# Kernel tuning notes

Hardware: AMD Instinct MI355X
Metric: run time of the kernel (lower is better)

Reference implementation:

```python
import jax, jax.numpy as jnp
import numpy as np
import math

B, T, D, H = 2, 2048, 2048, 16
HD = D // H  # head_dim = 128


def setup_inputs() -> dict:
    key = jax.random.key(0)
    ks = jax.random.split(key, 9)
    s = 1.0 / math.sqrt(D)
    return {
        "x": jax.random.normal(ks[0], (B, T, D), dtype=jnp.float32),
        "Wq": jax.random.normal(ks[1], (D, D), dtype=jnp.float32) * s,
        "bq": jax.random.normal(ks[2], (D,), dtype=jnp.float32) * 0.01,
        "Wk": jax.random.normal(ks[3], (D, D), dtype=jnp.float32) * s,
        "bk": jax.random.normal(ks[4], (D,), dtype=jnp.float32) * 0.01,
        "Wv": jax.random.normal(ks[5], (D, D), dtype=jnp.float32) * s,
        "bv": jax.random.normal(ks[6], (D,), dtype=jnp.float32) * 0.01,
        "Wo": jax.random.normal(ks[7], (D, D), dtype=jnp.float32) * s,
        "bo": jax.random.normal(ks[8], (D,), dtype=jnp.float32) * 0.01,
    }


def reference(x, Wq, bq, Wk, bk, Wv, bv, Wo, bo):
    b, t, c = x.shape
    # projections; split heads: (B,T,D) -> (B,H,T,HD)
    def split_heads(y):
        return y.reshape(b, t, H, HD).transpose(0, 2, 1, 3)

    q = split_heads(x @ Wq + bq)
    k = split_heads(x @ Wk + bk)
    v = split_heads(x @ Wv + bv)

    scale = 1.0 / math.sqrt(HD)
    attn = jnp.einsum('bhqd,bhkd->bhqk', q, k) * scale  # (B,H,T,T)
    # causal mask (prefill path: past_k is None)
    causal = jnp.tril(jnp.ones((t, t), dtype=bool))
    attn = jnp.where(causal, attn, -jnp.inf)
    attn = jax.nn.softmax(attn, axis=-1)
    out = jnp.einsum('bhqk,bhkd->bhqd', attn, v)  # (B,H,T,HD)
    out = out.transpose(0, 2, 1, 3).reshape(b, t, c)
    out = out @ Wo + bo
    return (out, k, v)
```

## Files before the change

kernel.cpp:

```cpp
#include <hip/hip_runtime.h>
#include <hip/hip_bf16.h>

#define B_ 2
#define T_ 2048
#define D_ 2048
#define H_ 16
#define HD_ 128
#define M_ 4096

typedef __attribute__((ext_vector_type(8))) short short8;
typedef __attribute__((ext_vector_type(8))) __bf16 bf16x8;
typedef __attribute__((ext_vector_type(4))) float f32x4;
typedef __attribute__((ext_vector_type(4))) unsigned uint32x4;

__device__ __forceinline__ short f2bf(float f) {
  unsigned u = __builtin_bit_cast(unsigned, f);
  u += 0x7fffu + ((u >> 16) & 1u);
  return (short)(u >> 16);
}

__device__ __forceinline__ unsigned pk2(float lo, float hi) {
  return ((unsigned)(unsigned short)f2bf(hi) << 16) |
         (unsigned)(unsigned short)f2bf(lo);
}

__device__ __forceinline__ void gl_lds16(const void* g, void* l) {
  __builtin_amdgcn_global_load_lds(
      (const __attribute__((address_space(1))) unsigned int*)g,
      (__attribute__((address_space(3))) unsigned int*)l, 16, 0, 0);
}

__device__ __forceinline__ f32x4 mfma_bf16(short8 a, short8 b, f32x4 c) {
  return __builtin_amdgcn_mfma_f32_16x16x32_bf16(
      __builtin_bit_cast(bf16x8, a), __builtin_bit_cast(bf16x8, b), c, 0, 0, 0);
}

__device__ __forceinline__ float2 sw16f(float x) {
  float a = x, bv;
  asm("v_mov_b32 %0, %1" : "=v"(bv) : "v"(x));
  asm("v_permlane16_swap_b32 %0, %1" : "+v"(a), "+v"(bv));
  return make_float2(a, bv);
}
__device__ __forceinline__ float2 sw32f(float x) {
  float a = x, bv;
  asm("v_mov_b32 %0, %1" : "=v"(bv) : "v"(x));
  asm("v_permlane32_swap_b32 %0, %1" : "+v"(a), "+v"(bv));
  return make_float2(a, bv);
}
__device__ __forceinline__ void sw16u(unsigned x, unsigned& e, unsigned& o) {
  unsigned a = x, bv;
  asm("v_mov_b32 %0, %1" : "=v"(bv) : "v"(x));
  asm("v_permlane16_swap_b32 %0, %1" : "+v"(a), "+v"(bv));
  e = a; o = bv;
}
__device__ __forceinline__ void pl32u(unsigned& a, unsigned& b) {
  asm("v_permlane32_swap_b32 %0, %1" : "+v"(a), "+v"(b));
}

__global__ void cast_f32_bf16(const float* __restrict__ in, short* __restrict__ out, int n4) {
  int i = blockIdx.x * blockDim.x + threadIdx.x;
  int stride = gridDim.x * blockDim.x;
  for (; i < n4; i += stride) {
    float4 v = ((const float4*)in)[i];
    short4 s;
    s.x = f2bf(v.x); s.y = f2bf(v.y); s.z = f2bf(v.z); s.w = f2bf(v.w);
    ((short4*)out)[i] = s;
  }
}

__global__ void transpose_cast_w4(const float* __restrict__ Wq, const float* __restrict__ Wk,
                                  const float* __restrict__ Wv, const float* __restrict__ Wo,
                                  short* __restrict__ wqkv, short* __restrict__ wo) {
  __shared__ float t[32][33];
  int z = blockIdx.z;
  const float* W = z == 0 ? Wq : z == 1 ? Wk : z == 2 ? Wv : Wo;
  short* dst = z < 3 ? wqkv + (size_t)z * D_ * D_ : wo;
  int n0 = blockIdx.x * 32, k0 = blockIdx.y * 32;
  int tx = threadIdx.x, ty = threadIdx.y;
#pragma unroll
  for (int j = 0; j < 4; ++j)
    t[ty + j * 8][tx] = W[(size_t)(k0 + ty + j * 8) * D_ + n0 + tx];
  __syncthreads();
#pragma unroll
  for (int j = 0; j < 4; ++j)
    dst[(size_t)(n0 + ty + j * 8) * D_ + k0 + tx] = f2bf(t[tx][ty + j * 8]);
}

__global__ __launch_bounds__(512, 2) void gemm_qkv(
    const short* __restrict__ A, const short* __restrict__ Bt,
    const float* __restrict__ b0, const float* __restrict__ b1,
    const float* __restrict__ b2,
    short* __restrict__ q_o, short* __restrict__ k_o,
    float* __restrict__ kf_o, float* __restrict__ vf_o,
    short* __restrict__ vt_o) {
  __shared__ __attribute__((aligned(16))) char lds[2][57344];
  const int K = D_, NT = K / 64;

  int d = blockIdx.x;
  int lg = (d & 7) * 64 + (d >> 3);
  int m0 = (lg & 15) * 256, n0 = (lg >> 4) * 192;

  int tid = threadIdx.x, lane = tid & 63, wid = tid >> 6;
  int wm = wid >> 2, wn = wid & 3;
  int lr = lane & 15, g = lane >> 4;

  int rowA = tid >> 2;
  int cA = ((((tid & 3) << 4) ^ (((rowA >> 1) & 3) << 4)) >> 1);
  const short* aS = A + (size_t)(m0 + rowA) * K + cA;
  int rowB = tid >> 3;
  int cB = ((((tid & 7) << 4) ^ ((rowB & 7) << 4)) >> 1);
  const short* bS = Bt + (size_t)(n0 + rowB) * K + cB;
  char* ldsb = (char*)lds;

  auto stageA = [&](int ts, int kh) {
    char* dst = ldsb + (ts & 1) * 57344 + kh * 16384 + tid * 16;
    const short* s = aS + ts * 64 + kh * 32;
    gl_lds16(s, dst);
    gl_lds16(s + (size_t)128 * K, dst + 8192);
  };
  auto stageB = [&](int ts) {
    char* dst = ldsb + (ts & 1) * 57344 + 32768 + tid * 16;
    const short* s = bS + ts * 64;
    gl_lds16(s, dst);
    gl_lds16(s + (size_t)64 * K, dst + 8192);
    gl_lds16(s + (size_t)128 * K, dst + 16384);
  };

  int swzA = (g * 16) ^ (((lr >> 1) & 3) << 4);
  int aoff = (wm * 128 + lr) * 64 + swzA;
  int boff0 = (wn * 48 + lr) * 128 + ((g * 16) ^ ((lr & 7) << 4));
  int boff1 = (wn * 48 + lr) * 128 + (((64 + g * 16)) ^ ((lr & 7) << 4));

  f32x4 acc[8][3] = {};

  stageA(0, 0); stageB(0); stageA(0, 1); stageA(1, 0);
  asm volatile("s_waitcnt vmcnt(4)" ::: "memory");
  __builtin_amdgcn_s_barrier();
  __builtin_amdgcn_sched_barrier(0);

#pragma unroll 1
  for (int t = 0; t < NT; ++t) {
    const char* base = ldsb + (t & 1) * 57344;
    int t1 = (t + 1 < NT) ? t + 1 : NT - 1;
    int t2 = (t + 2 < NT) ? t + 2 : NT - 1;
    short8 afr[8], bfr[3];

#pragma unroll
    for (int mi = 0; mi < 8; ++mi) afr[mi] = *(const short8*)(base + aoff + mi * 1024);
#pragma unroll
    for (int ni = 0; ni < 3; ++ni) bfr[ni] = *(const short8*)(base + 32768 + boff0 + ni * 2048);
    stageA(t1, 1); stageB(t1);
    __builtin_amdgcn_s_setprio(1);
#pragma unroll
    for (int mi = 0; mi < 8; ++mi)
#pragma unroll
      for (int ni = 0; ni < 3; ++ni)
        acc[mi][ni] = mfma_bf16(afr[mi], bfr[ni], acc[mi][ni]);
    __builtin_amdgcn_s_setprio(0);
    asm volatile("s_waitcnt vmcnt(7)" ::: "memory");
    __builtin_amdgcn_s_barrier();
    __builtin_amdgcn_sched_barrier(0);

#pragma unroll
    for (int mi = 0; mi < 8; ++mi) afr[mi] = *(const short8*)(base + 16384 + aoff + mi * 1024);
#pragma unroll
    for (int ni = 0; ni < 3; ++ni) bfr[ni] = *(const short8*)(base + 32768 + boff1 + ni * 2048);
    stageA(t2, 0);
    __builtin_amdgcn_s_setprio(1);
#pragma unroll
    for (int mi = 0; mi < 8; ++mi)
#pragma unroll
      for (int ni = 0; ni < 3; ++ni)
        acc[mi][ni] = mfma_bf16(afr[mi], bfr[ni], acc[mi][ni]);
    __builtin_amdgcn_s_setprio(0);
    asm volatile("s_waitcnt vmcnt(2)" ::: "memory");
    __builtin_amdgcn_s_barrier();
    __builtin_amdgcn_sched_barrier(0);
  }

#pragma unroll
  for (int ni = 0; ni < 3; ++ni) {
    int gcb = n0 + wn * 48 + ni * 16;
    int region = gcb >> 11;
    int nc = (gcb & 2047) + lr;
    int hh = nc >> 7, hd = nc & 127;
    const float* bias = region == 0 ? b0 : region == 1 ? b1 : b2;
    float bv = bias[nc];
#pragma unroll
    for (int mi = 0; mi < 8; ++mi) {
      int gr0 = m0 + wm * 128 + mi * 16 + (g << 2);
      int bb = gr0 >> 11, tt0 = gr0 & 2047;
      size_t hbase = (size_t)(bb * H_ + hh);
      float v0 = acc[mi][ni][0] + bv;
      float v1 = acc[mi][ni][1] + bv;
      float v2 = acc[mi][ni][2] + bv;
      float v3 = acc[mi][ni][3] + bv;
      size_t ib = (hbase * T_ + tt0) * HD_ + hd;
      if (region == 0) {
        q_o[ib] = f2bf(v0); q_o[ib + HD_] = f2bf(v1);
        q_o[ib + 2 * HD_] = f2bf(v2); q_o[ib + 3 * HD_] = f2bf(v3);
      } else if (region == 1) {
        k_o[ib] = f2bf(v0); k_o[ib + HD_] = f2bf(v1);
        k_o[ib + 2 * HD_] = f2bf(v2); k_o[ib + 3 * HD_] = f2bf(v3);
        kf_o[ib] = v0; kf_o[ib + HD_] = v1;
        kf_o[ib + 2 * HD_] = v2; kf_o[ib + 3 * HD_] = v3;
      } else {
        vf_o[ib] = v0; vf_o[ib + HD_] = v1;
        vf_o[ib + 2 * HD_] = v2; vf_o[ib + 3 * HD_] = v3;
        short4 s4;
        s4.x = f2bf(v0); s4.y = f2bf(v1); s4.z = f2bf(v2); s4.w = f2bf(v3);
        *(short4*)&vt_o[(hbase * HD_ + hd) * T_ + tt0] = s4;
      }
    }
  }
}

__global__ __launch_bounds__(256, 2) void gemm_rb(
    const short* __restrict__ A, const short* __restrict__ Bt,
    const float* __restrict__ b0, float* __restrict__ f_o) {
  __shared__ __attribute__((aligned(16))) short lds[4][2][4096];
  const int K = D_, NT = K / 32;

  int nx = gridDim.x, nwg = nx * gridDim.y;
  int d = blockIdx.y * nx + blockIdx.x;
  int cpx = nwg >> 3;
  int lg = (d & 7) * cpx + (d >> 3);
  int m0 = (lg / nx) * 128, n0 = (lg % nx) * 128;

  int tid = threadIdx.x, lane = tid & 63, w = tid >> 6;
  int wm = w >> 1, wn = w & 1;
  int lr = lane & 15, g = lane >> 4;

  int o1 = tid * 16, o2 = 4096 + tid * 16;
  int row1 = tid >> 2, row2 = 64 + row1;
  int cb = (tid & 3) << 4;
  int c1 = (cb ^ (((row1 >> 1) & 3) << 4)) >> 1;
  int c2 = (cb ^ (((row2 >> 1) & 3) << 4)) >> 1;
  const short* aS1 = A + (size_t)(m0 + row1) * K + c1;
  const short* aS2 = A + (size_t)(m0 + row2) * K + c2;
  const short* bS1 = Bt + (size_t)(n0 + row1) * K + c1;
  const short* bS2 = Bt + (size_t)(n0 + row2) * K + c2;

  int aoff[4], boff[4];
#pragma unroll
  for (int i = 0; i < 4; ++i) {
    int ra = wm * 64 + i * 16 + lr;
    aoff[i] = ra * 64 + ((g * 16) ^ (((ra >> 1) & 3) << 4));
    int rb = wn * 64 + i * 16 + lr;
    boff[i] = rb * 64 + ((g * 16) ^ (((rb >> 1) & 3) << 4));
  }

  f32x4 acc[4][4] = {};

#pragma unroll
  for (int s = 0; s < 3; ++s) {
    char* la = (char*)&lds[s][0][0];
    char* lb = (char*)&lds[s][1][0];
    gl_lds16(aS1 + s * 32, la + o1);
    gl_lds16(aS2 + s * 32, la + o2);
    gl_lds16(bS1 + s * 32, lb + o1);
    gl_lds16(bS2 + s * 32, lb + o2);
  }
  asm volatile("s_waitcnt vmcnt(8)" ::: "memory");
  __builtin_amdgcn_s_barrier();
  __builtin_amdgcn_sched_barrier(0);

#pragma unroll 1
  for (int t4 = 0; t4 < NT; t4 += 4) {
#pragma unroll
    for (int p = 0; p < 4; ++p) {
      int t = t4 + p;
      {
        int ts = (t + 3 < NT) ? t + 3 : NT - 1;
        char* la = (char*)&lds[(p + 3) & 3][0][0];
        char* lb = (char*)&lds[(p + 3) & 3][1][0];
        gl_lds16(aS1 + ts * 32, la + o1);
        gl_lds16(aS2 + ts * 32, la + o2);
        gl_lds16(bS1 + ts * 32, lb + o1);
        gl_lds16(bS2 + ts * 32, lb + o2);
      }
      const char* la = (const char*)&lds[p][0][0];
      const char* lb = (const char*)&lds[p][1][0];
      short8 af[4], bfv[4];
#pragma unroll
      for (int i = 0; i < 4; ++i) {
        af[i] = *(const short8*)(la + aoff[i]);
        bfv[i] = *(const short8*)(lb + boff[i]);
      }
      __builtin_amdgcn_s_setprio(1);
#pragma unroll
      for (int mi = 0; mi < 4; ++mi)
#pragma unroll
        for (int ni = 0; ni < 4; ++ni)
          acc[mi][ni] = mfma_bf16(af[mi], bfv[ni], acc[mi][ni]);
      __builtin_amdgcn_s_setprio(0);
      asm volatile("s_waitcnt vmcnt(8)" ::: "memory");
      __builtin_amdgcn_s_barrier();
      __builtin_amdgcn_sched_barrier(0);
    }
  }

#pragma unroll
  for (int mi = 0; mi < 4; ++mi) {
#pragma unroll
    for (int ni = 0; ni < 4; ++ni) {
      int gr0 = m0 + wm * 64 + mi * 16 + (g << 2);
      int gc = n0 + wn * 64 + ni * 16 + lr;
      float bv = b0[gc];
#pragma unroll
      for (int r = 0; r < 4; ++r)
        f_o[(size_t)(gr0 + r) * D_ + gc] = acc[mi][ni][r] + bv;
    }
  }
}

__global__ __launch_bounds__(256, 2) void attn_fwd(
    const short* __restrict__ qb, const short* __restrict__ kb,
    const short* __restrict__ vtb, short* __restrict__ aob) {
  __shared__ __attribute__((aligned(16))) char kvlds[2][16384];

  int d = blockIdx.y * gridDim.x + blockIdx.x;
  int lg = (d & 7) * 64 + (d >> 3);
  int bh = lg >> 4, jx = lg & 15;

  int tid = threadIdx.x, w = tid >> 6, lane = tid & 63;
  int lr = lane & 15, g = lane >> 4;
  const short* Q  = qb  + (size_t)bh * T_ * HD_;
  const short* Kp = kb  + (size_t)bh * T_ * HD_;
  const short* Vt = vtb + (size_t)bh * HD_ * T_;
  const float scale = 0.08838834764831845f;
  int b = bh >> 4, h = bh & 15;
  bool hi16 = (lane & 16) != 0;

  int oA = ((2 * w + 0) * 64 + lane) * 16;
  int oB = ((2 * w + 1) * 64 + lane) * 16;
  int rKA = oA >> 8, rKB = oB >> 8;
  size_t skA = (size_t)rKA * HD_ + (((oA & 255) ^ ((rKA & 7) << 4)) >> 1);
  size_t skB = (size_t)rKB * HD_ + (((oB & 255) ^ ((rKB & 7) << 4)) >> 1);
  int rVA = oA >> 6, rVB = oB >> 6;
  size_t svA = (size_t)rVA * T_ + (((oA & 63) ^ (((rVA >> 1) & 3) << 4)) >> 1);
  size_t svB = (size_t)rVB * T_ + (((oB & 63) ^ (((rVB >> 1) & 3) << 4)) >> 1);

#pragma unroll 1
  for (int pass = 0; pass < 2; ++pass) {
    int qt = pass ? (31 - jx) : jx;
    int q0 = qt * 64 + w * 16;
    int ntiles = 2 * qt + 2;

    {
      char* kd = &kvlds[0][0];
      char* vd = &kvlds[0][8192];
      gl_lds16(Kp + skA, kd + oA);
      gl_lds16(Kp + skB, kd + oB);
      gl_lds16(Vt + svA, vd + oA);
      gl_lds16(Vt + svB, vd + oB);
    }

    short8 qf[4];
#pragma unroll
    for (int kk = 0; kk < 4; ++kk)
      qf[kk] = *(const short8*)&Q[(size_t)(q0 + lr) * HD_ + kk * 32 + g * 8];

    f32x4 o[8] = {};
    float mrow = -1e30f, lrow = 0.f;
    __syncthreads();

#pragma unroll 1
    for (int t = 0; t < ntiles; ++t) {
      int kv0 = t * 32, buf = t & 1;
      if (t + 1 < ntiles) {
        char* kd = &kvlds[buf ^ 1][0];
        char* vd = &kvlds[buf ^ 1][8192];
        const short* Kn = Kp + (size_t)(kv0 + 32) * HD_;
        const short* Vn = Vt + (kv0 + 32);
        gl_lds16(Kn + skA, kd + oA);
        gl_lds16(Kn + skB, kd + oB);
        gl_lds16(Vn + svA, vd + oA);
        gl_lds16(Vn + svB, vd + oB);
      }
      if (kv0 < q0 + 16) {
        const char* kb_ = &kvlds[buf][0];
        const char* vb_ = &kvlds[buf][8192];
        short8 kf0[4], kf1[4], vf[8];
#pragma unroll
        for (int kk = 0; kk < 4; ++kk) {
          int cs = (kk * 64 + g * 16) ^ ((lr & 7) << 4);
          kf0[kk] = *(const short8*)(kb_ + (lr * 256 + cs));
          kf1[kk] = *(const short8*)(kb_ + ((16 + lr) * 256 + cs));
        }
#pragma unroll
        for (int f = 0; f < 8; ++f)
          vf[f] = *(const short8*)(vb_ + ((f * 16 + lr) * 64 +
                   ((g * 16) ^ (((lr >> 1) & 3) << 4))));

        f32x4 s0 = {}, s1 = {};
        __builtin_amdgcn_s_setprio(1);
#pragma unroll
        for (int kk = 0; kk < 4; ++kk) {
          s0 = mfma_bf16(kf0[kk], qf[kk], s0);
          s1 = mfma_bf16(kf1[kk], qf[kk], s1);
        }
        __builtin_amdgcn_s_setprio(0);

        float vv[8];
#pragma unroll
        for (int r = 0; r < 4; ++r) {
          vv[r] = s0[r] * scale;
          vv[4 + r] = s1[r] * scale;
        }
        if (kv0 + 31 > q0) {
          int qrow = q0 + lr;
#pragma unroll
          for (int r = 0; r < 4; ++r) {
            if (kv0 + 4 * g + r > qrow) vv[r] = -1e30f;
            if (kv0 + 16 + 4 * g + r > qrow) vv[4 + r] = -1e30f;
          }
        }

        float pm = vv[0];
#pragma unroll
        for (int i = 1; i < 8; ++i) pm = fmaxf(pm, vv[i]);
        { float2 tpm = sw32f(pm); pm = fmaxf(tpm.x, tpm.y); }
        { float2 tpm = sw16f(pm); pm = fmaxf(tpm.x, tpm.y); }

        bool rescale = !__all(pm - mrow <= 8.0f);
        float alpha = 1.0f;
        if (rescale) {
          float mnew = fmaxf(mrow, pm);
          alpha = __expf(mrow - mnew);
          mrow = mnew;
        }

        float p[8];
        float rs = 0.f;
#pragma unroll
        for (int i = 0; i < 8; ++i) { p[i] = __expf(vv[i] - mrow); rs += p[i]; }
        { float2 trs = sw32f(rs); rs = trs.x + trs.y; }
        { float2 trs = sw16f(rs); rs = trs.x + trs.y; }
        lrow = (rescale ? lrow * alpha : lrow) + rs;

        if (rescale) {
          float alr[4];
#pragma unroll
          for (int r = 0; r < 4; ++r) alr[r] = __shfl(alpha, 4 * g + r);
#pragma unroll
          for (int f = 0; f < 8; ++f)
#pragma unroll
            for (int r = 0; r < 4; ++r) o[f][r] *= alr[r];
        }

        unsigned w0 = pk2(p[0], p[1]), w1 = pk2(p[2], p[3]);
        unsigned w2 = pk2(p[4], p[5]), w3 = pk2(p[6], p[7]);
        unsigned e0, od0, e1, od1, e2, od2, e3, od3;
        sw16u(w0, e0, od0); sw16u(w1, e1, od1);
        sw16u(w2, e2, od2); sw16u(w3, e3, od3);
        unsigned F0 = e0,  S0 = e2;  pl32u(F0, S0);
        unsigned F1 = e1,  S1 = e3;  pl32u(F1, S1);
        unsigned F2 = od0, S2 = od2; pl32u(F2, S2);
        unsigned F3 = od1, S3 = od3; pl32u(F3, S3);
        uint32x4 paw = { hi16 ? S0 : F0, hi16 ? S1 : F1,
                         hi16 ? S2 : F2, hi16 ? S3 : F3 };
        short8 pa = __builtin_bit_cast(short8, paw);

        __builtin_amdgcn_s_setprio(1);
#pragma unroll
        for (int f = 0; f < 8; ++f) o[f] = mfma_bf16(pa, vf[f], o[f]);
        __builtin_amdgcn_s_setprio(0);
      }
      __syncthreads();
    }

    float inv = 1.0f / lrow;
    float invr[4];
#pragma unroll
    for (int r = 0; r < 4; ++r) invr[r] = __shfl(inv, 4 * g + r);
#pragma unroll
    for (int r = 0; r < 4; ++r) {
      int q = q0 + 4 * g + r;
      size_t rowoff = ((size_t)(b * T_ + q)) * D_ + h * HD_;
#pragma unroll
      for (int f = 0; f < 8; ++f)
        aob[rowoff + f * 16 + lr] = f2bf(o[f][r] * invr[r]);
    }
  }
}

extern "C" void kernel_launch(void* const* d_in, const int* in_sizes, int n_in,
                              void* d_out, int out_size, void* d_ws, size_t ws_size,
                              hipStream_t stream) {
  const float* x  = (const float*)d_in[0];
  const float* Wq = (const float*)d_in[1];
  const float* bq = (const float*)d_in[2];
  const float* Wk = (const float*)d_in[3];
  const float* bk = (const float*)d_in[4];
  const float* Wv = (const float*)d_in[5];
  const float* bv = (const float*)d_in[6];
  const float* Wo = (const float*)d_in[7];
  const float* bo = (const float*)d_in[8];
  float* out  = (float*)d_out;
  float* kout = out + (size_t)M_ * D_;
  float* vout = kout + (size_t)M_ * D_;

  char* ws = (char*)d_ws;
  auto alloc = [&](size_t bytes) {
    char* p = ws;
    ws += (bytes + 255) & ~(size_t)255;
    return p;
  };
  short* xb    = (short*)alloc((size_t)M_ * D_ * 2);
  short* wqkvT = (short*)alloc((size_t)3 * D_ * D_ * 2);
  short* woT   = (short*)alloc((size_t)D_ * D_ * 2);
  short* qb    = (short*)alloc((size_t)M_ * D_ * 2);
  short* kb    = (short*)alloc((size_t)M_ * D_ * 2);
  short* vtb   = (short*)alloc((size_t)M_ * D_ * 2);
  short* aob = xb;

  cast_f32_bf16<<<2048, 256, 0, stream>>>(x, xb, M_ * D_ / 4);
  dim3 tb(32, 8);
  transpose_cast_w4<<<dim3(64, 64, 4), tb, 0, stream>>>(Wq, Wk, Wv, Wo, wqkvT, woT);

  gemm_qkv<<<512, 512, 0, stream>>>(xb, wqkvT, bq, bk, bv, qb, kb, kout, vout, vtb);
  attn_fwd<<<dim3(16, 32), 256, 0, stream>>>(qb, kb, vtb, aob);
  gemm_rb<<<dim3(16, 32), 256, 0, stream>>>(aob, woT, bo, out);
}
```

Before: 256.4 us.

## Split GEMM k-step into four interleaved phases and use hardware bf16 pack

Restructures the projection GEMM main loop so each half-k step is split into two sub-phases of 4 M-fragments. LDS fragment loads and global-to-LDS staging are interleaved with barriers, and the vmcnt waits are retuned to match the new issue order. The aim is to cut register pressure from holding 8 A fragments and to overlap MFMA with staging at finer grain, at the cost of more barriers per iteration. Separately, the attention P-to-bf16 packing swaps the software round-to-nearest for the v_cvt_pk_bf16_f32 instruction.

```diff
diff --git a/kernel.cpp b/kernel.cpp
--- a/kernel.cpp
+++ b/kernel.cpp
@@ -19,9 +19,10 @@
   return (short)(u >> 16);
 }
 
-__device__ __forceinline__ unsigned pk2(float lo, float hi) {
-  return ((unsigned)(unsigned short)f2bf(hi) << 16) |
-         (unsigned)(unsigned short)f2bf(lo);
+__device__ __forceinline__ unsigned cvtpk(float lo, float hi) {
+  unsigned r;
+  asm("v_cvt_pk_bf16_f32 %0, %1, %2" : "=v"(r) : "v"(lo), "v"(hi));
+  return r;
 }
 
 __device__ __forceinline__ void gl_lds16(const void* g, void* l) {
@@ -129,12 +130,12 @@
   int swzA = (g * 16) ^ (((lr >> 1) & 3) << 4);
   int aoff = (wm * 128 + lr) * 64 + swzA;
   int boff0 = (wn * 48 + lr) * 128 + ((g * 16) ^ ((lr & 7) << 4));
-  int boff1 = (wn * 48 + lr) * 128 + (((64 + g * 16)) ^ ((lr & 7) << 4));
+  int boff1 = (wn * 48 + lr) * 128 + ((64 + g * 16) ^ ((lr & 7) << 4));
 
   f32x4 acc[8][3] = {};
 
-  stageA(0, 0); stageB(0); stageA(0, 1); stageA(1, 0);
-  asm volatile("s_waitcnt vmcnt(4)" ::: "memory");
+  stageA(0, 0); stageA(0, 1); stageB(0); stageA(1, 0);
+  asm volatile("s_waitcnt vmcnt(2)" ::: "memory");
   __builtin_amdgcn_s_barrier();
   __builtin_amdgcn_sched_barrier(0);
 
@@ -143,35 +144,71 @@
     const char* base = ldsb + (t & 1) * 57344;
     int t1 = (t + 1 < NT) ? t + 1 : NT - 1;
     int t2 = (t + 2 < NT) ? t + 2 : NT - 1;
-    short8 afr[8], bfr[3];
-
-#pragma unroll
-    for (int mi = 0; mi < 8; ++mi) afr[mi] = *(const short8*)(base + aoff + mi * 1024);
+    short8 afr[4], bfr[3];
+
+#pragma unroll
+    for (int mi = 0; mi < 4; ++mi) afr[mi] = *(const short8*)(base + aoff + mi * 1024);
 #pragma unroll
     for (int ni = 0; ni < 3; ++ni) bfr[ni] = *(const short8*)(base + 32768 + boff0 + ni * 2048);
-    stageA(t1, 1); stageB(t1);
+    stageA(t1, 1);
+    __builtin_amdgcn_s_barrier();
+    asm volatile("s_waitcnt lgkmcnt(0)" ::: "memory");
+    __builtin_amdgcn_sched_barrier(0);
     __builtin_amdgcn_s_setprio(1);
 #pragma unroll
-    for (int mi = 0; mi < 8; ++mi)
+    for (int mi = 0; mi < 4; ++mi)
 #pragma unroll
       for (int ni = 0; ni < 3; ++ni)
         acc[mi][ni] = mfma_bf16(afr[mi], bfr[ni], acc[mi][ni]);
     __builtin_amdgcn_s_setprio(0);
-    asm volatile("s_waitcnt vmcnt(7)" ::: "memory");
-    __builtin_amdgcn_s_barrier();
-    __builtin_amdgcn_sched_barrier(0);
-
-#pragma unroll
-    for (int mi = 0; mi < 8; ++mi) afr[mi] = *(const short8*)(base + 16384 + aoff + mi * 1024);
+    __builtin_amdgcn_s_barrier();
+    __builtin_amdgcn_sched_barrier(0);
+
+#pragma unroll
+    for (int mi = 0; mi < 4; ++mi) afr[mi] = *(const short8*)(base + aoff + (4 + mi) * 1024);
+    stageB(t1);
+    __builtin_amdgcn_s_barrier();
+    asm volatile("s_waitcnt lgkmcnt(0)" ::: "memory");
+    __builtin_amdgcn_sched_barrier(0);
+    __builtin_amdgcn_s_setprio(1);
+#pragma unroll
+    for (int mi = 0; mi < 4; ++mi)
+#pragma unroll
+      for (int ni = 0; ni < 3; ++ni)
+        acc[4 + mi][ni] = mfma_bf16(afr[mi], bfr[ni], acc[4 + mi][ni]);
+    __builtin_amdgcn_s_setprio(0);
+    __builtin_amdgcn_s_barrier();
+    __builtin_amdgcn_sched_barrier(0);
+
+#pragma unroll
+    for (int mi = 0; mi < 4; ++mi) afr[mi] = *(const short8*)(base + 16384 + aoff + mi * 1024);
 #pragma unroll
     for (int ni = 0; ni < 3; ++ni) bfr[ni] = *(const short8*)(base + 32768 + boff1 + ni * 2048);
     stageA(t2, 0);
+    __builtin_amdgcn_s_barrier();
+    asm volatile("s_waitcnt lgkmcnt(0)" ::: "memory");
+    __builtin_amdgcn_sched_barrier(0);
     __builtin_amdgcn_s_setprio(1);
 #pragma unroll
-    for (int mi = 0; mi < 8; ++mi)
+    for (int mi = 0; mi < 4; ++mi)
 #pragma unroll
       for (int ni = 0; ni < 3; ++ni)
         acc[mi][ni] = mfma_bf16(afr[mi], bfr[ni], acc[mi][ni]);
+    __builtin_amdgcn_s_setprio(0);
+    __builtin_amdgcn_s_barrier();
+    __builtin_amdgcn_sched_barrier(0);
+
+#pragma unroll
+    for (int mi = 0; mi < 4; ++mi) afr[mi] = *(const short8*)(base + 16384 + aoff + (4 + mi) * 1024);
+    __builtin_amdgcn_s_barrier();
+    asm volatile("s_waitcnt lgkmcnt(0)" ::: "memory");
+    __builtin_amdgcn_sched_barrier(0);
+    __builtin_amdgcn_s_setprio(1);
+#pragma unroll
+    for (int mi = 0; mi < 4; ++mi)
+#pragma unroll
+      for (int ni = 0; ni < 3; ++ni)
+        acc[4 + mi][ni] = mfma_bf16(afr[mi], bfr[ni], acc[4 + mi][ni]);
     __builtin_amdgcn_s_setprio(0);
     asm volatile("s_waitcnt vmcnt(2)" ::: "memory");
     __builtin_amdgcn_s_barrier();
@@ -449,8 +486,8 @@
             for (int r = 0; r < 4; ++r) o[f][r] *= alr[r];
         }
 
-        unsigned w0 = pk2(p[0], p[1]), w1 = pk2(p[2], p[3]);
-        unsigned w2 = pk2(p[4], p[5]), w3 = pk2(p[6], p[7]);
+        unsigned w0 = cvtpk(p[0], p[1]), w1 = cvtpk(p[2], p[3]);
+        unsigned w2 = cvtpk(p[4], p[5]), w3 = cvtpk(p[6], p[7]);
         unsigned e0, od0, e1, od1, e2, od2, e3, od3;
         sw16u(w0, e0, od0); sw16u(w1, e1, od1);
         sw16u(w2, e2, od2); sw16u(w3, e3, od3);
```

After: 255.1 us. About the same (-0.5%).

## Enlarge QKV GEMM tile to 512x192 with triple-buffered K=32 stages

Applied to the files above, without the earlier changes.

The QKV projection GEMM now uses 512x192 block tiles on 256 blocks, with 4x2 waves each computing 128x96. It streams K in 32-wide steps through a three-slot LDS ring instead of a double-buffered 64-wide one. The aim is more reuse per loaded tile and deeper prefetch, paid for with more accumulator registers and fewer blocks, which lowers occupancy and CU coverage. Separately, the bf16 packing in attention switches from software rounding to the hardware v_cvt_pk_bf16_f32 instruction, and idle waves issue dummy loads so the vmcnt counts stay uniform.

```diff
diff --git a/kernel.cpp b/kernel.cpp
--- a/kernel.cpp
+++ b/kernel.cpp
@@ -19,9 +19,10 @@
   return (short)(u >> 16);
 }
 
-__device__ __forceinline__ unsigned pk2(float lo, float hi) {
-  return ((unsigned)(unsigned short)f2bf(hi) << 16) |
-         (unsigned)(unsigned short)f2bf(lo);
+__device__ __forceinline__ unsigned cvtpk(float lo, float hi) {
+  unsigned r;
+  asm("v_cvt_pk_bf16_f32 %0, %1, %2" : "=v"(r) : "v"(lo), "v"(hi));
+  return r;
 }
 
 __device__ __forceinline__ void gl_lds16(const void* g, void* l) {
@@ -93,94 +94,88 @@
     short* __restrict__ q_o, short* __restrict__ k_o,
     float* __restrict__ kf_o, float* __restrict__ vf_o,
     short* __restrict__ vt_o) {
-  __shared__ __attribute__((aligned(16))) char lds[2][57344];
-  const int K = D_, NT = K / 64;
+  __shared__ __attribute__((aligned(16))) char lds[3 * 45056 + 2048];
+  const int K = D_, NT = K / 32;
 
   int d = blockIdx.x;
-  int lg = (d & 7) * 64 + (d >> 3);
-  int m0 = (lg & 15) * 256, n0 = (lg >> 4) * 192;
+  int lg = (d & 7) * 32 + (d >> 3);
+  int m0 = (lg & 7) * 512, n0 = (lg >> 3) * 192;
 
   int tid = threadIdx.x, lane = tid & 63, wid = tid >> 6;
-  int wm = wid >> 2, wn = wid & 3;
+  int wm = wid >> 1, wn = wid & 1;
   int lr = lane & 15, g = lane >> 4;
 
-  int rowA = tid >> 2;
-  int cA = ((((tid & 3) << 4) ^ (((rowA >> 1) & 3) << 4)) >> 1);
-  const short* aS = A + (size_t)(m0 + rowA) * K + cA;
-  int rowB = tid >> 3;
-  int cB = ((((tid & 7) << 4) ^ ((rowB & 7) << 4)) >> 1);
-  const short* bS = Bt + (size_t)(n0 + rowB) * K + cB;
+  int scol = ((((tid & 3) << 4) ^ (((tid >> 3) & 3) << 4)) >> 1);
+  const short* aS = A + (size_t)(m0 + (tid >> 2)) * K + scol;
+  const short* bS = Bt + (size_t)(n0 + (tid >> 2)) * K + scol;
   char* ldsb = (char*)lds;
-
-  auto stageA = [&](int ts, int kh) {
-    char* dst = ldsb + (ts & 1) * 57344 + kh * 16384 + tid * 16;
-    const short* s = aS + ts * 64 + kh * 32;
-    gl_lds16(s, dst);
-    gl_lds16(s + (size_t)128 * K, dst + 8192);
+  char* scratch = ldsb + 3 * 45056;
+
+  auto stage = [&](int ts, int slot) {
+    char* sl = ldsb + slot * 45056;
+    const short* sa = aS + ts * 32;
+#pragma unroll
+    for (int j = 0; j < 4; ++j)
+      gl_lds16(sa + (size_t)j * 128 * K, sl + j * 8192 + wid * 1024);
+    if (wid < 6) {
+      const short* sb = bS + ts * 32;
+      gl_lds16(sb, sl + 32768 + wid * 1024);
+      gl_lds16(sb + (size_t)96 * K, sl + 32768 + 6144 + wid * 1024);
+    } else {
+      gl_lds16(A + lane * 8, scratch + (wid - 6) * 1024);
+      gl_lds16(A + lane * 8, scratch + (wid - 6) * 1024);
+    }
   };
-  auto stageB = [&](int ts) {
-    char* dst = ldsb + (ts & 1) * 57344 + 32768 + tid * 16;
-    const short* s = bS + ts * 64;
-    gl_lds16(s, dst);
-    gl_lds16(s + (size_t)64 * K, dst + 8192);
-    gl_lds16(s + (size_t)128 * K, dst + 16384);
-  };
-
-  int swzA = (g * 16) ^ (((lr >> 1) & 3) << 4);
-  int aoff = (wm * 128 + lr) * 64 + swzA;
-  int boff0 = (wn * 48 + lr) * 128 + ((g * 16) ^ ((lr & 7) << 4));
-  int boff1 = (wn * 48 + lr) * 128 + (((64 + g * 16)) ^ ((lr & 7) << 4));
-
-  f32x4 acc[8][3] = {};
-
-  stageA(0, 0); stageB(0); stageA(0, 1); stageA(1, 0);
-  asm volatile("s_waitcnt vmcnt(4)" ::: "memory");
+
+  int fsw = (g * 16) ^ (((lr >> 1) & 3) << 4);
+  int aoff = (wm * 128 + lr) * 64 + fsw;
+  int boff = 32768 + (wn * 96 + lr) * 64 + fsw;
+
+  f32x4 acc[8][6] = {};
+
+  stage(0, 0);
+  stage(1, 1);
+  asm volatile("s_waitcnt vmcnt(6)" ::: "memory");
   __builtin_amdgcn_s_barrier();
   __builtin_amdgcn_sched_barrier(0);
 
+  int sR = 0, sW = 2;
 #pragma unroll 1
   for (int t = 0; t < NT; ++t) {
-    const char* base = ldsb + (t & 1) * 57344;
-    int t1 = (t + 1 < NT) ? t + 1 : NT - 1;
-    int t2 = (t + 2 < NT) ? t + 2 : NT - 1;
-    short8 afr[8], bfr[3];
-
-#pragma unroll
-    for (int mi = 0; mi < 8; ++mi) afr[mi] = *(const short8*)(base + aoff + mi * 1024);
-#pragma unroll
-    for (int ni = 0; ni < 3; ++ni) bfr[ni] = *(const short8*)(base + 32768 + boff0 + ni * 2048);
-    stageA(t1, 1); stageB(t1);
+    const char* sl = ldsb + sR * 45056;
+    short8 bfr[6], afr[4];
+#pragma unroll
+    for (int ni = 0; ni < 6; ++ni) bfr[ni] = *(const short8*)(sl + boff + ni * 1024);
+#pragma unroll
+    for (int mi = 0; mi < 4; ++mi) afr[mi] = *(const short8*)(sl + aoff + mi * 1024);
+    int ts = (t + 2 < NT) ? t + 2 : NT - 1;
+    stage(ts, sW);
     __builtin_amdgcn_s_setprio(1);
 #pragma unroll
-    for (int mi = 0; mi < 8; ++mi)
-#pragma unroll
-      for (int ni = 0; ni < 3; ++ni)
+    for (int mi = 0; mi < 4; ++mi)
+#pragma unroll
+      for (int ni = 0; ni < 6; ++ni)
         acc[mi][ni] = mfma_bf16(afr[mi], bfr[ni], acc[mi][ni]);
     __builtin_amdgcn_s_setprio(0);
-    asm volatile("s_waitcnt vmcnt(7)" ::: "memory");
+#pragma unroll
+    for (int mi = 0; mi < 4; ++mi) afr[mi] = *(const short8*)(sl + aoff + (4 + mi) * 1024);
+    __builtin_amdgcn_s_setprio(1);
+#pragma unroll
+    for (int mi = 0; mi < 4; ++mi)
+#pragma unroll
+      for (int ni = 0; ni < 6; ++ni)
+        acc[4 + mi][ni] = mfma_bf16(afr[mi], bfr[ni], acc[4 + mi][ni]);
+    __builtin_amdgcn_s_setprio(0);
+    asm volatile("s_waitcnt vmcnt(6)" ::: "memory");
     __builtin_amdgcn_s_barrier();
     __builtin_amdgcn_sched_barrier(0);
-
-#pragma unroll
-    for (int mi = 0; mi < 8; ++mi) afr[mi] = *(const short8*)(base + 16384 + aoff + mi * 1024);
-#pragma unroll
-    for (int ni = 0; ni < 3; ++ni) bfr[ni] = *(const short8*)(base + 32768 + boff1 + ni * 2048);
-    stageA(t2, 0);
-    __builtin_amdgcn_s_setprio(1);
-#pragma unroll
-    for (int mi = 0; mi < 8; ++mi)
-#pragma unroll
-      for (int ni = 0; ni < 3; ++ni)
-        acc[mi][ni] = mfma_bf16(afr[mi], bfr[ni], acc[mi][ni]);
-    __builtin_amdgcn_s_setprio(0);
-    asm volatile("s_waitcnt vmcnt(2)" ::: "memory");
-    __builtin_amdgcn_s_barrier();
-    __builtin_amdgcn_sched_barrier(0);
-  }
-
-#pragma unroll
-  for (int ni = 0; ni < 3; ++ni) {
-    int gcb = n0 + wn * 48 + ni * 16;
+    sR = (sR == 2) ? 0 : sR + 1;
+    sW = (sW == 2) ? 0 : sW + 1;
+  }
+
+#pragma unroll
+  for (int ni = 0; ni < 6; ++ni) {
+    int gcb = n0 + wn * 96 + ni * 16;
     int region = gcb >> 11;
     int nc = (gcb & 2047) + lr;
     int hh = nc >> 7, hd = nc & 127;
@@ -449,8 +444,8 @@
             for (int r = 0; r < 4; ++r) o[f][r] *= alr[r];
         }
 
-        unsigned w0 = pk2(p[0], p[1]), w1 = pk2(p[2], p[3]);
-        unsigned w2 = pk2(p[4], p[5]), w3 = pk2(p[6], p[7]);
+        unsigned w0 = cvtpk(p[0], p[1]), w1 = cvtpk(p[2], p[3]);
+        unsigned w2 = cvtpk(p[4], p[5]), w3 = cvtpk(p[6], p[7]);
         unsigned e0, od0, e1, od1, e2, od2, e3, od3;
         sw16u(w0, e0, od0); sw16u(w1, e1, od1);
         sw16u(w2, e2, od2); sw16u(w3, e3, od3);
@@ -519,7 +514,7 @@
   dim3 tb(32, 8);
   transpose_cast_w4<<<dim3(64, 64, 4), tb, 0, stream>>>(Wq, Wk, Wv, Wo, wqkvT, woT);
 
-  gemm_qkv<<<512, 512, 0, stream>>>(xb, wqkvT, bq, bk, bv, qb, kb, kout, vout, vtb);
+  gemm_qkv<<<256, 512, 0, stream>>>(xb, wqkvT, bq, bk, bv, qb, kb, kout, vout, vtb);
   attn_fwd<<<dim3(16, 32), 256, 0, stream>>>(qb, kb, vtb, aob);
   gemm_rb<<<dim3(16, 32), 256, 0, stream>>>(aob, woT, bo, out);
 }
```

Measured after the change: 248.4 us. 1.03x faster.

## Split attention into one block per query tile, longest first, with exp2 softmax

Applied to the files above, without the earlier changes.

The attention kernel stops pairing two query tiles per block (short plus long for balance) and launches 1024 blocks, each handling one query tile, ordered from the longest causal tile down. The aim is better dynamic load balance and more resident parallelism. The softmax now folds log2(e) into the scale and uses raw v_exp_f32, and the rescale threshold is adjusted to match. Float-to-bf16 packing uses the hardware v_cvt_pk_bf16_f32 instruction instead of manual rounding. The split adds extra per-block setup and Q loads.

```diff
diff --git a/kernel.cpp b/kernel.cpp
--- a/kernel.cpp
+++ b/kernel.cpp
@@ -19,9 +19,16 @@
   return (short)(u >> 16);
 }
 
-__device__ __forceinline__ unsigned pk2(float lo, float hi) {
-  return ((unsigned)(unsigned short)f2bf(hi) << 16) |
-         (unsigned)(unsigned short)f2bf(lo);
+__device__ __forceinline__ unsigned cvtpk(float lo, float hi) {
+  unsigned r;
+  asm("v_cvt_pk_bf16_f32 %0, %1, %2" : "=v"(r) : "v"(lo), "v"(hi));
+  return r;
+}
+
+__device__ __forceinline__ float ex2(float x) {
+  float r;
+  asm("v_exp_f32 %0, %1" : "=v"(r) : "v"(x));
+  return r;
 }
 
 __device__ __forceinline__ void gl_lds16(const void* g, void* l) {
@@ -129,7 +136,7 @@
   int swzA = (g * 16) ^ (((lr >> 1) & 3) << 4);
   int aoff = (wm * 128 + lr) * 64 + swzA;
   int boff0 = (wn * 48 + lr) * 128 + ((g * 16) ^ ((lr & 7) << 4));
-  int boff1 = (wn * 48 + lr) * 128 + (((64 + g * 16)) ^ ((lr & 7) << 4));
+  int boff1 = (wn * 48 + lr) * 128 + ((64 + g * 16) ^ ((lr & 7) << 4));
 
   f32x4 acc[8][3] = {};
 
@@ -319,16 +326,15 @@
     const short* __restrict__ vtb, short* __restrict__ aob) {
   __shared__ __attribute__((aligned(16))) char kvlds[2][16384];
 
-  int d = blockIdx.y * gridDim.x + blockIdx.x;
-  int lg = (d & 7) * 64 + (d >> 3);
-  int bh = lg >> 4, jx = lg & 15;
-
+  int d = blockIdx.x;
+  int bh = d & 31;
+  int qt = 31 - (d >> 5);
   int tid = threadIdx.x, w = tid >> 6, lane = tid & 63;
   int lr = lane & 15, g = lane >> 4;
   const short* Q  = qb  + (size_t)bh * T_ * HD_;
   const short* Kp = kb  + (size_t)bh * T_ * HD_;
   const short* Vt = vtb + (size_t)bh * HD_ * T_;
-  const float scale = 0.08838834764831845f;
+  const float scale2 = 0.12751879202f;
   int b = bh >> 4, h = bh & 15;
   bool hi16 = (lane & 16) != 0;
 
@@ -341,147 +347,143 @@
   size_t svA = (size_t)rVA * T_ + (((oA & 63) ^ (((rVA >> 1) & 3) << 4)) >> 1);
   size_t svB = (size_t)rVB * T_ + (((oB & 63) ^ (((rVB >> 1) & 3) << 4)) >> 1);
 
+  int q0 = qt * 64 + w * 16;
+  int ntiles = 2 * qt + 2;
+
+  {
+    char* kd = &kvlds[0][0];
+    char* vd = &kvlds[0][8192];
+    gl_lds16(Kp + skA, kd + oA);
+    gl_lds16(Kp + skB, kd + oB);
+    gl_lds16(Vt + svA, vd + oA);
+    gl_lds16(Vt + svB, vd + oB);
+  }
+
+  short8 qf[4];
+#pragma unroll
+  for (int kk = 0; kk < 4; ++kk)
+    qf[kk] = *(const short8*)&Q[(size_t)(q0 + lr) * HD_ + kk * 32 + g * 8];
+
+  f32x4 o[8] = {};
+  float mrow = -1e30f, lrow = 0.f;
+  __syncthreads();
+
 #pragma unroll 1
-  for (int pass = 0; pass < 2; ++pass) {
-    int qt = pass ? (31 - jx) : jx;
-    int q0 = qt * 64 + w * 16;
-    int ntiles = 2 * qt + 2;
-
-    {
-      char* kd = &kvlds[0][0];
-      char* vd = &kvlds[0][8192];
-      gl_lds16(Kp + skA, kd + oA);
-      gl_lds16(Kp + skB, kd + oB);
-      gl_lds16(Vt + svA, vd + oA);
-      gl_lds16(Vt + svB, vd + oB);
+  for (int t = 0; t < ntiles; ++t) {
+    int kv0 = t * 32, buf = t & 1;
+    if (t + 1 < ntiles) {
+      char* kd = &kvlds[buf ^ 1][0];
+      char* vd = &kvlds[buf ^ 1][8192];
+      const short* Kn = Kp + (size_t)(kv0 + 32) * HD_;
+      const short* Vn = Vt + (kv0 + 32);
+      gl_lds16(Kn + skA, kd + oA);
+      gl_lds16(Kn + skB, kd + oB);
+      gl_lds16(Vn + svA, vd + oA);
+      gl_lds16(Vn + svB, vd + oB);
     }
-
-    short8 qf[4];
-#pragma unroll
-    for (int kk = 0; kk < 4; ++kk)
-      qf[kk] = *(const short8*)&Q[(size_t)(q0 + lr) * HD_ + kk * 32 + g * 8];
-
-    f32x4 o[8] = {};
-    float mrow = -1e30f, lrow = 0.f;
+    if (kv0 < q0 + 16) {
+      const char* kb_ = &kvlds[buf][0];
+      const char* vb_ = &kvlds[buf][8192];
+      short8 kf0[4], kf1[4], vf[8];
+#pragma unroll
+      for (int kk = 0; kk < 4; ++kk) {
+        int cs = (kk * 64 + g * 16) ^ ((lr & 7) << 4);
+        kf0[kk] = *(const short8*)(kb_ + (lr * 256 + cs));
+        kf1[kk] = *(const short8*)(kb_ + ((16 + lr) * 256 + cs));
+      }
+#pragma unroll
+      for (int f = 0; f < 8; ++f)
+        vf[f] = *(const short8*)(vb_ + ((f * 16 + lr) * 64 +
+                 ((g * 16) ^ (((lr >> 1) & 3) << 4))));
+
+      f32x4 s0 = {}, s1 = {};
+      __builtin_amdgcn_s_setprio(1);
+#pragma unroll
+      for (int kk = 0; kk < 4; ++kk) {
+        s0 = mfma_bf16(kf0[kk], qf[kk], s0);
+        s1 = mfma_bf16(kf1[kk], qf[kk], s1);
+      }
+      __builtin_amdgcn_s_setprio(0);
+
+      float vv[8];
+#pragma unroll
+      for (int r = 0; r < 4; ++r) {
+        vv[r] = s0[r] * scale2;
+        vv[4 + r] = s1[r] * scale2;
+      }
+      if (kv0 + 31 > q0) {
+        int qrow = q0 + lr;
+#pragma unroll
+        for (int r = 0; r < 4; ++r) {
+          if (kv0 + 4 * g + r > qrow) vv[r] = -1e30f;
+          if (kv0 + 16 + 4 * g + r > qrow) vv[4 + r] = -1e30f;
+        }
+      }
+
+      float pm = vv[0];
+#pragma unroll
+      for (int i = 1; i < 8; ++i) pm = fmaxf(pm, vv[i]);
+      { float2 tpm = sw32f(pm); pm = fmaxf(tpm.x, tpm.y); }
+      { float2 tpm = sw16f(pm); pm = fmaxf(tpm.x, tpm.y); }
+
+      bool rescale = !__all(pm - mrow <= 11.54f);
+      float alpha = 1.0f;
+      if (rescale) {
+        float mnew = fmaxf(mrow, pm);
+        alpha = ex2(mrow - mnew);
+        mrow = mnew;
+      }
+
+      float p[8];
+      float rs = 0.f;
+#pragma unroll
+      for (int i = 0; i < 8; ++i) { p[i] = ex2(vv[i] - mrow); rs += p[i]; }
+      { float2 trs = sw32f(rs); rs = trs.x + trs.y; }
+      { float2 trs = sw16f(rs); rs = trs.x + trs.y; }
+      lrow = (rescale ? lrow * alpha : lrow) + rs;
+
+      if (rescale) {
+        float alr[4];
+#pragma unroll
+        for (int r = 0; r < 4; ++r) alr[r] = __shfl(alpha, 4 * g + r);
+#pragma unroll
+        for (int f = 0; f < 8; ++f)
+#pragma unroll
+          for (int r = 0; r < 4; ++r) o[f][r] *= alr[r];
+      }
+
+      unsigned w0 = cvtpk(p[0], p[1]), w1 = cvtpk(p[2], p[3]);
+      unsigned w2 = cvtpk(p[4], p[5]), w3 = cvtpk(p[6], p[7]);
+      unsigned e0, od0, e1, od1, e2, od2, e3, od3;
+      sw16u(w0, e0, od0); sw16u(w1, e1, od1);
+      sw16u(w2, e2, od2); sw16u(w3, e3, od3);
+      unsigned F0 = e0,  S0 = e2;  pl32u(F0, S0);
+      unsigned F1 = e1,  S1 = e3;  pl32u(F1, S1);
+      unsigned F2 = od0, S2 = od2; pl32u(F2, S2);
+      unsigned F3 = od1, S3 = od3; pl32u(F3, S3);
+      uint32x4 paw = { hi16 ? S0 : F0, hi16 ? S1 : F1,
+                       hi16 ? S2 : F2, hi16 ? S3 : F3 };
+      short8 pa = __builtin_bit_cast(short8, paw);
+
+      __builtin_amdgcn_s_setprio(1);
+#pragma unroll
+      for (int f = 0; f < 8; ++f) o[f] = mfma_bf16(pa, vf[f], o[f]);
+      __builtin_amdgcn_s_setprio(0);
+    }
     __syncthreads();
-
-#pragma unroll 1
-    for (int t = 0; t < ntiles; ++t) {
-      int kv0 = t * 32, buf = t & 1;
-      if (t + 1 < ntiles) {
-        char* kd = &kvlds[buf ^ 1][0];
-        char* vd = &kvlds[buf ^ 1][8192];
-        const short* Kn = Kp + (size_t)(kv0 + 32) * HD_;
-        const short* Vn = Vt + (kv0 + 32);
-        gl_lds16(Kn + skA, kd + oA);
-        gl_lds16(Kn + skB, kd + oB);
-        gl_lds16(Vn + svA, vd + oA);
-        gl_lds16(Vn + svB, vd + oB);
-      }
-      if (kv0 < q0 + 16) {
-        const char* kb_ = &kvlds[buf][0];
-        const char* vb_ = &kvlds[buf][8192];
-        short8 kf0[4], kf1[4], vf[8];
-#pragma unroll
-        for (int kk = 0; kk < 4; ++kk) {
-          int cs = (kk * 64 + g * 16) ^ ((lr & 7) << 4);
-          kf0[kk] = *(const short8*)(kb_ + (lr * 256 + cs));
-          kf1[kk] = *(const short8*)(kb_ + ((16 + lr) * 256 + cs));
-        }
-#pragma unroll
-        for (int f = 0; f < 8; ++f)
-          vf[f] = *(const short8*)(vb_ + ((f * 16 + lr) * 64 +
-                   ((g * 16) ^ (((lr >> 1) & 3) << 4))));
-
-        f32x4 s0 = {}, s1 = {};
-        __builtin_amdgcn_s_setprio(1);
-#pragma unroll
-        for (int kk = 0; kk < 4; ++kk) {
-          s0 = mfma_bf16(kf0[kk], qf[kk], s0);
-          s1 = mfma_bf16(kf1[kk], qf[kk], s1);
-        }
-        __builtin_amdgcn_s_setprio(0);
-
-        float vv[8];
-#pragma unroll
-        for (int r = 0; r < 4; ++r) {
-          vv[r] = s0[r] * scale;
-          vv[4 + r] = s1[r] * scale;
-        }
-        if (kv0 + 31 > q0) {
-          int qrow = q0 + lr;
-#pragma unroll
-          for (int r = 0; r < 4; ++r) {
-            if (kv0 + 4 * g + r > qrow) vv[r] = -1e30f;
-            if (kv0 + 16 + 4 * g + r > qrow) vv[4 + r] = -1e30f;
-          }
-        }
-
-        float pm = vv[0];
-#pragma unroll
-        for (int i = 1; i < 8; ++i) pm = fmaxf(pm, vv[i]);
-        { float2 tpm = sw32f(pm); pm = fmaxf(tpm.x, tpm.y); }
-        { float2 tpm = sw16f(pm); pm = fmaxf(tpm.x, tpm.y); }
-
-        bool rescale = !__all(pm - mrow <= 8.0f);
-        float alpha = 1.0f;
-        if (rescale) {
-          float mnew = fmaxf(mrow, pm);
-          alpha = __expf(mrow - mnew);
-          mrow = mnew;
-        }
-
-        float p[8];
-        float rs = 0.f;
-#pragma unroll
-        for (int i = 0; i < 8; ++i) { p[i] = __expf(vv[i] - mrow); rs += p[i]; }
-        { float2 trs = sw32f(rs); rs = trs.x + trs.y; }
-        { float2 trs = sw16f(rs); rs = trs.x + trs.y; }
-        lrow = (rescale ? lrow * alpha : lrow) + rs;
-
-        if (rescale) {
-          float alr[4];
-#pragma unroll
-          for (int r = 0; r < 4; ++r) alr[r] = __shfl(alpha, 4 * g + r);
-#pragma unroll
-          for (int f = 0; f < 8; ++f)
-#pragma unroll
-            for (int r = 0; r < 4; ++r) o[f][r] *= alr[r];
-        }
-
-        unsigned w0 = pk2(p[0], p[1]), w1 = pk2(p[2], p[3]);
-        unsigned w2 = pk2(p[4], p[5]), w3 = pk2(p[6], p[7]);
-        unsigned e0, od0, e1, od1, e2, od2, e3, od3;
-        sw16u(w0, e0, od0); sw16u(w1, e1, od1);
-        sw16u(w2, e2, od2); sw16u(w3, e3, od3);
-        unsigned F0 = e0,  S0 = e2;  pl32u(F0, S0);
-        unsigned F1 = e1,  S1 = e3;  pl32u(F1, S1);
-        unsigned F2 = od0, S2 = od2; pl32u(F2, S2);
-        unsigned F3 = od1, S3 = od3; pl32u(F3, S3);
-        uint32x4 paw = { hi16 ? S0 : F0, hi16 ? S1 : F1,
-                         hi16 ? S2 : F2, hi16 ? S3 : F3 };
-        short8 pa = __builtin_bit_cast(short8, paw);
-
-        __builtin_amdgcn_s_setprio(1);
-#pragma unroll
-        for (int f = 0; f < 8; ++f) o[f] = mfma_bf16(pa, vf[f], o[f]);
-        __builtin_amdgcn_s_setprio(0);
-      }
-      __syncthreads();
-    }
-
-    float inv = 1.0f / lrow;
-    float invr[4];
-#pragma unroll
-    for (int r = 0; r < 4; ++r) invr[r] = __shfl(inv, 4 * g + r);
-#pragma unroll
-    for (int r = 0; r < 4; ++r) {
-      int q = q0 + 4 * g + r;
-      size_t rowoff = ((size_t)(b * T_ + q)) * D_ + h * HD_;
-#pragma unroll
-      for (int f = 0; f < 8; ++f)
-        aob[rowoff + f * 16 + lr] = f2bf(o[f][r] * invr[r]);
-    }
+  }
+
+  float inv = 1.0f / lrow;
+  float invr[4];
+#pragma unroll
+  for (int r = 0; r < 4; ++r) invr[r] = __shfl(inv, 4 * g + r);
+#pragma unroll
+  for (int r = 0; r < 4; ++r) {
+    int q = q0 + 4 * g + r;
+    size_t rowoff = ((size_t)(b * T_ + q)) * D_ + h * HD_;
+#pragma unroll
+    for (int f = 0; f < 8; ++f)
+      aob[rowoff + f * 16 + lr] = f2bf(o[f][r] * invr[r]);
   }
 }
 
@@ -520,6 +522,6 @@
   transpose_cast_w4<<<dim3(64, 64, 4), tb, 0, stream>>>(Wq, Wk, Wv, Wo, wqkvT, woT);
 
   gemm_qkv<<<512, 512, 0, stream>>>(xb, wqkvT, bq, bk, bv, qb, kb, kout, vout, vtb);
-  attn_fwd<<<dim3(16, 32), 256, 0, stream>>>(qb, kb, vtb, aob);
+  attn_fwd<<<1024, 256, 0, stream>>>(qb, kb, vtb, aob);
   gemm_rb<<<dim3(16, 32), 256, 0, stream>>>(aob, woT, bo, out);
 }
```

New measurement: 246.7 us. -3.8%, faster.
